# Optimization experiments

Measured on AMD Instinct MI355X. Metric: run time of the kernel, lower is better.

Reference implementation:

```python
import jax, jax.numpy as jnp
import numpy as np

# Config matching init_kwargs: layer_nb=1 -> stride 16, image 608x608 -> 38x38 grid
B, CIN, H, W = 32, 512, 38, 38
NA, NC = 3, 80
STRIDE = 16.0
ANCHORS = np.array([[30.0, 61.0], [62.0, 45.0], [59.0, 119.0]], dtype=np.float32)


def setup_inputs() -> dict:
    key = jax.random.key(0)
    k1, k2, k3 = jax.random.split(key, 3)
    xin = jax.random.normal(k1, (B, CIN, H, W), dtype=jnp.float32)
    # 1x1 conv weight stored as (out_ch, in_ch); out_ch = NA*(NC+5) = 255
    conv_w = jax.random.normal(k2, (NA * (NC + 5), CIN), dtype=jnp.float32) * 0.02
    conv_b = jax.random.normal(k3, (NA * (NC + 5),), dtype=jnp.float32) * 0.01
    return {"xin": xin, "conv_w": conv_w, "conv_b": conv_b}


def reference(xin, conv_w, conv_b):
    # 1x1 conv == channel GEMM; fuse the NCHW->NHWC permute into the einsum
    fm = jnp.einsum('bchw,oc->bhwo', xin, conv_w) + conv_b  # [B,H,W,255]
    fm = fm.reshape(B, H, W, NA, NC + 5)
    tx, ty, tw, th = fm[..., 0], fm[..., 1], fm[..., 2], fm[..., 3]
    # grid offsets (precomputed via broadcasting instead of per-call numpy rebuild)
    x_off = jnp.arange(W, dtype=fm.dtype)[None, None, :, None]   # broadcast over B,H,NA
    y_off = jnp.arange(H, dtype=fm.dtype)[None, :, None, None]   # broadcast over B,W,NA
    anchors = jnp.asarray(ANCHORS, dtype=fm.dtype)               # [NA,2]
    bx = (jax.nn.sigmoid(tx) + x_off) * STRIDE
    by = (jax.nn.sigmoid(ty) + y_off) * STRIDE
    bw = jnp.exp(tw) * anchors[:, 0]
    bh = jnp.exp(th) * anchors[:, 1]
    boxes = jnp.stack([bx, by, bw, bh], axis=-1)                 # [B,H,W,NA,4]
    # concat decoded boxes with raw objectness + class logits -> [B,H,W,NA,85]
    return jnp.concatenate([boxes, fm[..., 4:]], axis=-1)
```

## Files before the change

### kernel.cpp

```cpp
#include <hip/hip_runtime.h>
#include <hip/hip_bf16.h>
#include <cstdint>
#include <cstddef>

#define CIN_K  512
#define WW_    38
#define BHW    1444
#define NOUT   255
#define MTOT   46208

#define BM     64
#define EP_DW  260

typedef __attribute__((ext_vector_type(8))) short  bf16x8;
typedef __attribute__((ext_vector_type(4))) float  floatx4;

static __device__ __forceinline__ unsigned f2bf(float f) {
    unsigned u = __builtin_bit_cast(unsigned, f);
    return (u + 0x7FFFu + ((u >> 16) & 1u)) >> 16;
}

static __device__ __forceinline__ unsigned pk2bf(float a, float b) {
    __hip_bfloat162 h = __float22bfloat162_rn(make_float2(a, b));
    unsigned r;
    __builtin_memcpy(&r, &h, 4);
    return r;
}

__global__ void conv_w_to_bf16(const float* __restrict__ cw,
                               unsigned short* __restrict__ wb) {
    int tg   = blockIdx.x * 256 + threadIdx.x;
    int base = tg * 8;
    int n    = base >> 9;
    unsigned rr[4] = {0u, 0u, 0u, 0u};
    if (n < NOUT) {
        float4 v0 = *(const float4*)(cw + base);
        float4 v1 = *(const float4*)(cw + base + 4);
        rr[0] = f2bf(v0.x) | (f2bf(v0.y) << 16);
        rr[1] = f2bf(v0.z) | (f2bf(v0.w) << 16);
        rr[2] = f2bf(v1.x) | (f2bf(v1.y) << 16);
        rr[3] = f2bf(v1.z) | (f2bf(v1.w) << 16);
    }
    *(uint4*)(wb + base) = *(uint4*)rr;
}

__global__ __launch_bounds__(256, 3)
void yolo_head(const float* __restrict__ xin,
               const unsigned short* __restrict__ wb,
               const float* __restrict__ cb,
               float* __restrict__ out)
{
    __shared__ unsigned smem[32 * EP_DW];

    const int t    = threadIdx.x;
    const int w    = t >> 6;
    const int lane = t & 63;
    const int l15  = lane & 15;
    const int q    = lane >> 4;

    const int orig = blockIdx.x;
    const int xcd  = orig & 7;
    const int rank = orig >> 3;
    const int wgid = (xcd < 2 ? xcd * 91 : 182 + (xcd - 2) * 90) + rank;
    const int m0   = wgid * BM;

    const float* pa[4];
#pragma unroll
    for (int i = 0; i < 4; ++i) {
        int m  = m0 + i * 16 + l15;
        int bi = m / BHW;
        int hw = m - bi * BHW;
        pa[i] = xin + (size_t)bi * (CIN_K * BHW) + hw + (size_t)(q * 8) * BHW;
    }

    floatx4 acc[4][4];
#pragma unroll
    for (int i = 0; i < 4; ++i)
#pragma unroll
        for (int j = 0; j < 4; ++j)
            acc[i][j] = (floatx4){0.f, 0.f, 0.f, 0.f};

    const unsigned short* pbw = wb + (size_t)(w * 64 + l15) * CIN_K + q * 8;

#pragma unroll
    for (int kc = 0; kc < 16; ++kc) {
        bf16x8 bfr[4], af[4];
#pragma unroll
        for (int j = 0; j < 4; ++j) {
            uint4 bv = *(const uint4*)(pbw + (size_t)j * 16 * CIN_K + kc * 32);
            bfr[j] = __builtin_bit_cast(bf16x8, bv);
        }
#pragma unroll
        for (int i = 0; i < 4; ++i) {
            float a8[8];
#pragma unroll
            for (int u = 0; u < 8; ++u)
                a8[u] = pa[i][(size_t)(kc * 32 + u) * BHW];
            unsigned d[4];
#pragma unroll
            for (int e = 0; e < 4; ++e)
                d[e] = pk2bf(a8[2 * e], a8[2 * e + 1]);
            af[i] = __builtin_bit_cast(bf16x8, *(uint4*)d);
        }
#pragma unroll
        for (int i = 0; i < 4; ++i)
#pragma unroll
            for (int j = 0; j < 4; ++j)
                acc[i][j] = __builtin_amdgcn_mfma_f32_16x16x32_bf16(
                                af[i], bfr[j], acc[i][j], 0, 0, 0);
    }

#pragma unroll
    for (int j = 0; j < 4; ++j) {
        int   n    = w * 64 + j * 16 + l15;
        int   nc   = n < NOUT ? n : NOUT - 1;
        int   ai   = nc / 85;
        int   ji   = nc - ai * 85;
        float bias = cb[nc];
        float aw   = (ai == 0) ? 30.f : (ai == 1) ? 62.f : 59.f;
        float ah   = (ai == 0) ? 61.f : (ai == 1) ? 45.f : 119.f;
#pragma unroll
        for (int i = 0; i < 4; ++i)
#pragma unroll
            for (int r = 0; r < 4; ++r) {
                int   md  = m0 + i * 16 + q * 4 + r;
                int   rem = md % BHW;
                int   hh  = rem / WW_;
                float v   = acc[i][j][r] + bias;
                float res;
                if (ji == 0)      res = (1.f / (1.f + __expf(-v)) + (float)(rem - hh * WW_)) * 16.f;
                else if (ji == 1) res = (1.f / (1.f + __expf(-v)) + (float)hh) * 16.f;
                else if (ji == 2) res = __expf(v) * aw;
                else if (ji == 3) res = __expf(v) * ah;
                else              res = v;
                acc[i][j][r] = res;
            }
    }

    float* EP = (float*)smem;
#pragma unroll
    for (int p = 0; p < 2; ++p) {
        __syncthreads();
#pragma unroll
        for (int i2 = 0; i2 < 2; ++i2) {
            const int i = p * 2 + i2;
#pragma unroll
            for (int j = 0; j < 4; ++j)
#pragma unroll
                for (int r = 0; r < 4; ++r)
                    EP[(i2 * 16 + q * 4 + r) * EP_DW + w * 64 + j * 16 + l15] =
                        acc[i][j][r];
        }
        __syncthreads();

        const float* EPb = (const float*)smem + (w * 8) * EP_DW;
        float*       ob  = out + (size_t)(m0 + p * 32 + w * 8) * NOUT;
#pragma unroll
        for (int s2 = 0; s2 < 8; ++s2) {
            int f4 = s2 * 64 + lane;
            if (f4 < 510) {
                int   f = f4 * 4;
                float vs[4];
#pragma unroll
                for (int e = 0; e < 4; ++e) {
                    int fe = f + e;
                    int mr = fe / NOUT;
                    int x  = fe - mr * NOUT;
                    vs[e]  = EPb[mr * EP_DW + x];
                }
                *(float4*)(ob + f) = make_float4(vs[0], vs[1], vs[2], vs[3]);
            }
        }
    }
}

extern "C" void kernel_launch(void* const* d_in, const int* in_sizes, int n_in,
                              void* d_out, int out_size, void* d_ws, size_t ws_size,
                              hipStream_t stream) {
    const float* xin = (const float*)d_in[0];
    const float* cw  = (const float*)d_in[1];
    const float* cb  = (const float*)d_in[2];
    float*       out = (float*)d_out;
    unsigned short* wb = (unsigned short*)d_ws;

    hipLaunchKernelGGL(conv_w_to_bf16, dim3(64), dim3(256), 0, stream, cw, wb);
    hipLaunchKernelGGL(yolo_head, dim3(MTOT / BM), dim3(256), 0, stream,
                       xin, wb, cb, out);
}
```

Baseline: 210.8 us.

## Stage activation tiles through double-buffered LDS with vectorized prefetch loads

The A operand is now loaded in K chunks of 128 with float4 global loads into registers, converted to bf16 and written into a double-buffered LDS tile. MFMA fragments are then read from LDS. The next chunk's global loads are issued while the current chunk is being computed. This replaces the per-lane scalar loads strided by BHW and is meant to cut load instruction count and hide global latency. The cost is extra LDS traffic and barriers per chunk, plus higher LDS use that may limit occupancy.

```diff
diff --git a/kernel.cpp b/kernel.cpp
--- a/kernel.cpp
+++ b/kernel.cpp
@@ -10,6 +10,9 @@
 #define MTOT   46208
 
 #define BM     64
+#define KCH    128
+#define ROWE   132
+#define CH_DW  (64 * 66)
 #define EP_DW  260
 
 typedef __attribute__((ext_vector_type(8))) short  bf16x8;
@@ -50,7 +53,9 @@
                const float* __restrict__ cb,
                float* __restrict__ out)
 {
-    __shared__ unsigned smem[32 * EP_DW];
+    __shared__ unsigned smem[2 * CH_DW];
+    unsigned short* As0 = (unsigned short*)smem;
+    unsigned short* As1 = (unsigned short*)(smem + CH_DW);
 
     const int t    = threadIdx.x;
     const int w    = t >> 6;
@@ -64,14 +69,33 @@
     const int wgid = (xcd < 2 ? xcd * 91 : 182 + (xcd - 2) * 90) + rank;
     const int m0   = wgid * BM;
 
-    const float* pa[4];
-#pragma unroll
-    for (int i = 0; i < 4; ++i) {
-        int m  = m0 + i * 16 + l15;
-        int bi = m / BHW;
-        int hw = m - bi * BHW;
-        pa[i] = xin + (size_t)bi * (CIN_K * BHW) + hw + (size_t)(q * 8) * BHW;
-    }
+    const int mq4 = (t & 15) * 4;
+    const int kq4 = (t >> 4) * 4;
+    const int m4  = m0 + mq4;
+    const int bi  = m4 / BHW;
+    const int hw  = m4 - bi * BHW;
+    const float* pb0 = xin + (size_t)bi * (CIN_K * BHW) + hw;
+
+    alignas(16) float P[2][4][4];
+
+    auto LOADREG = [&](int c) {
+#pragma unroll
+        for (int s = 0; s < 2; ++s)
+#pragma unroll
+            for (int kk = 0; kk < 4; ++kk)
+                *(float4*)&P[s][kk][0] =
+                    *(const float4*)(pb0 + (size_t)(c * KCH + s * 64 + kq4 + kk) * BHW);
+    };
+    auto PACKWRITE = [&](unsigned short* dst) {
+#pragma unroll
+        for (int s = 0; s < 2; ++s)
+#pragma unroll
+            for (int r = 0; r < 4; ++r) {
+                unsigned lo = pk2bf(P[s][0][r], P[s][1][r]);
+                unsigned hi = pk2bf(P[s][2][r], P[s][3][r]);
+                *(uint2*)(&dst[(mq4 + r) * ROWE + s * 64 + kq4]) = make_uint2(lo, hi);
+            }
+    };
 
     floatx4 acc[4][4];
 #pragma unroll
@@ -82,32 +106,46 @@
 
     const unsigned short* pbw = wb + (size_t)(w * 64 + l15) * CIN_K + q * 8;
 
-#pragma unroll
-    for (int kc = 0; kc < 16; ++kc) {
-        bf16x8 bfr[4], af[4];
-#pragma unroll
-        for (int j = 0; j < 4; ++j) {
-            uint4 bv = *(const uint4*)(pbw + (size_t)j * 16 * CIN_K + kc * 32);
-            bfr[j] = __builtin_bit_cast(bf16x8, bv);
-        }
-#pragma unroll
-        for (int i = 0; i < 4; ++i) {
-            float a8[8];
-#pragma unroll
-            for (int u = 0; u < 8; ++u)
-                a8[u] = pa[i][(size_t)(kc * 32 + u) * BHW];
-            unsigned d[4];
-#pragma unroll
-            for (int e = 0; e < 4; ++e)
-                d[e] = pk2bf(a8[2 * e], a8[2 * e + 1]);
-            af[i] = __builtin_bit_cast(bf16x8, *(uint4*)d);
-        }
-#pragma unroll
-        for (int i = 0; i < 4; ++i)
-#pragma unroll
-            for (int j = 0; j < 4; ++j)
-                acc[i][j] = __builtin_amdgcn_mfma_f32_16x16x32_bf16(
-                                af[i], bfr[j], acc[i][j], 0, 0, 0);
+    auto COMPUTE = [&](const unsigned short* src, int c) {
+#pragma unroll
+        for (int kc = 0; kc < 4; ++kc) {
+            bf16x8 bfr[4], af[4];
+#pragma unroll
+            for (int j = 0; j < 4; ++j) {
+                uint4 bv = *(const uint4*)(pbw + (size_t)j * 16 * CIN_K
+                                           + c * KCH + kc * 32);
+                bfr[j] = __builtin_bit_cast(bf16x8, bv);
+            }
+#pragma unroll
+            for (int i = 0; i < 4; ++i) {
+                int4 av = *(const int4*)(&src[(i * 16 + l15) * ROWE + kc * 32 + q * 8]);
+                af[i] = __builtin_bit_cast(bf16x8, av);
+            }
+#pragma unroll
+            for (int i = 0; i < 4; ++i)
+#pragma unroll
+                for (int j = 0; j < 4; ++j)
+                    acc[i][j] = __builtin_amdgcn_mfma_f32_16x16x32_bf16(
+                                    af[i], bfr[j], acc[i][j], 0, 0, 0);
+        }
+    };
+
+    LOADREG(0);
+    PACKWRITE(As0);
+    LOADREG(1);
+    __syncthreads();
+
+#pragma unroll
+    for (int c = 0; c < 4; ++c) {
+        const unsigned short* cur = (c & 1) ? As1 : As0;
+        unsigned short*       nxt = (c & 1) ? As0 : As1;
+        COMPUTE(cur, c);
+        if (c < 3) {
+            __syncthreads();
+            PACKWRITE(nxt);
+            __syncthreads();
+            if (c < 2) LOADREG(c + 2);
+        }
     }
 
 #pragma unroll
```

New measurement: 182.2 us. 1.16x faster.
